# Optimization experiments

Hardware: AMD Instinct MI355X
Metric: run time of the kernel (lower is better)

## Reference

```python
import jax, jax.numpy as jnp
import numpy as np

DIM = 512
HEADS = 8
DIM_HEAD = 64
INNER = HEADS * DIM_HEAD  # 512
SCALE = DIM_HEAD ** -0.5
LN_EPS = 1e-5


def setup_inputs() -> dict:
    key = jax.random.key(0)
    k1, k2, k3, k4 = jax.random.split(key, 4)
    b, p, n = 4, 64, 256
    x = jax.random.normal(k1, (b, p, n, DIM), dtype=jnp.float32)
    ln_g = jnp.ones((DIM,), jnp.float32)
    ln_b = jnp.zeros((DIM,), jnp.float32)
    # stored as [in, out] for x @ W
    w_qkv = jax.random.normal(k2, (DIM, 3 * INNER), jnp.float32) * (DIM ** -0.5)
    w_out = jax.random.normal(k3, (INNER, DIM), jnp.float32) * (INNER ** -0.5)
    b_out = jnp.zeros((DIM,), jnp.float32)
    return {"x": x, "ln_g": ln_g, "ln_b": ln_b, "w_qkv": w_qkv,
            "w_out": w_out, "b_out": b_out}


def reference(x, ln_g, ln_b, w_qkv, w_out, b_out):
    b, p, n, _ = x.shape
    # LayerNorm over last dim
    mu = jnp.mean(x, axis=-1, keepdims=True)
    var = jnp.mean(jnp.square(x - mu), axis=-1, keepdims=True)
    xn = (x - mu) * jax.lax.rsqrt(var + LN_EPS) * ln_g + ln_b
    # QKV projection (no bias)
    qkv = xn @ w_qkv                                   # [b,p,n,3*INNER]
    q, k, v = jnp.split(qkv, 3, axis=-1)
    def to_heads(t):
        return t.reshape(b, p, n, HEADS, DIM_HEAD).transpose(0, 1, 3, 2, 4)
    q, k, v = to_heads(q), to_heads(k), to_heads(v)    # [b,p,h,n,d]
    dots = jnp.einsum('bphnd,bphmd->bphnm', q, k) * SCALE
    attn = jax.nn.softmax(dots, axis=-1)
    out = jnp.einsum('bphnm,bphmd->bphnd', attn, v)    # [b,p,h,n,d]
    out = out.transpose(0, 1, 3, 2, 4).reshape(b, p, n, INNER)
    return out @ w_out + b_out
```

## Files before the change

kernel.cpp:

```cpp
#include <hip/hip_runtime.h>
#include <stdint.h>

#define DIMD 512
#define HEADS 8
#define DHEAD 64
#define NSEQ 256
#define NGRP 256
#define NROWS (NGRP * NSEQ)
#define TRIPLE 1536
#define ATT_SCALE 0.125f

typedef float f32x4 __attribute__((ext_vector_type(4)));
typedef _Float16 half8 __attribute__((ext_vector_type(8)));
typedef _Float16 half4 __attribute__((ext_vector_type(4)));

#define GLD16(gp, lp) __builtin_amdgcn_global_load_lds( \
    (const __attribute__((address_space(1))) void*)(gp), \
    (__attribute__((address_space(3))) void*)(lp), 16, 0, 0)

__global__ __launch_bounds__(256) void k_wconv(const float* __restrict__ wq,
                                               const float* __restrict__ wo,
                                               _Float16* __restrict__ wtq,
                                               _Float16* __restrict__ wto) {
  int id = blockIdx.x * 256 + threadIdx.x;
  if (id < DIMD * TRIPLE) {
    int k = id / TRIPLE, n = id % TRIPLE;
    wtq[n * DIMD + k] = (_Float16)wq[id];
  } else {
    int j = id - DIMD * TRIPLE;
    int k = j / DIMD, n = j % DIMD;
    wto[n * DIMD + k] = (_Float16)wo[j];
  }
}

__global__ __launch_bounds__(256) void k_ln(const float* __restrict__ x,
                                            const float* __restrict__ g,
                                            const float* __restrict__ b,
                                            _Float16* __restrict__ xn) {
  int row = blockIdx.x * 4 + (threadIdx.x >> 6);
  int lane = threadIdx.x & 63;
  const float* xr = x + (size_t)row * DIMD + lane * 8;
  float v[8];
  *(f32x4*)(v)     = *(const f32x4*)(xr);
  *(f32x4*)(v + 4) = *(const f32x4*)(xr + 4);
  float s = 0.f, ss = 0.f;
#pragma unroll
  for (int j = 0; j < 8; ++j) { s += v[j]; ss += v[j] * v[j]; }
#pragma unroll
  for (int m = 1; m < 64; m <<= 1) { s += __shfl_xor(s, m); ss += __shfl_xor(ss, m); }
  float mean = s * (1.f / DIMD);
  float var  = ss * (1.f / DIMD) - mean * mean;
  float rstd = rsqrtf(var + 1e-5f);
  const float* gp = g + lane * 8;
  const float* bp = b + lane * 8;
  half8 o;
#pragma unroll
  for (int j = 0; j < 8; ++j) o[j] = (_Float16)((v[j] - mean) * rstd * gp[j] + bp[j]);
  *(half8*)(xn + (size_t)row * DIMD + lane * 8) = o;
}

template <int N, int LDA, bool WITH_BIAS>
__global__ __launch_bounds__(256, 2) void k_gemm(const _Float16* __restrict__ A,
                                                 const _Float16* __restrict__ BT,
                                                 _Float16* __restrict__ Ch,
                                                 float* __restrict__ Cf,
                                                 const float* __restrict__ bias) {
  constexpr int NT = N / 128;
  int mt = blockIdx.x / NT, nt = blockIdx.x % NT;
  int m0 = mt * 128, n0 = nt * 128;
  int tid = threadIdx.x, lane = tid & 63, w = tid >> 6;
  int wr = w >> 1, wc = w & 1;
  int l15 = lane & 15, lg = lane >> 4;
  __shared__ _Float16 Asm[128 * 64];
  __shared__ _Float16 Bsm[128 * 64];
  f32x4 acc[4][4] = {};
  const int rA = lane >> 3;
  const int cA = (lane & 7) * 8;

  for (int ks = 0; ks < 8; ++ks) {
    int k0 = ks * 64;
#pragma unroll
    for (int i = 0; i < 4; ++i) {
      int r0 = w * 32 + i * 8;
      GLD16(A  + (size_t)(m0 + r0 + rA) * LDA + k0 + cA, &Asm[r0 * 64]);
      GLD16(BT + (size_t)(n0 + r0 + rA) * 512 + k0 + cA, &Bsm[r0 * 64]);
    }
    __syncthreads();
#pragma unroll
    for (int kk = 0; kk < 2; ++kk) {
      int co = kk * 32 + lg * 8;
      half8 a[4], b[4];
#pragma unroll
      for (int m = 0; m < 4; ++m) a[m] = *(const half8*)&Asm[(wr * 64 + m * 16 + l15) * 64 + co];
#pragma unroll
      for (int n = 0; n < 4; ++n) b[n] = *(const half8*)&Bsm[(wc * 64 + n * 16 + l15) * 64 + co];
#pragma unroll
      for (int m = 0; m < 4; ++m)
#pragma unroll
        for (int n = 0; n < 4; ++n)
          acc[m][n] = __builtin_amdgcn_mfma_f32_16x16x32_f16(a[m], b[n], acc[m][n], 0, 0, 0);
    }
    __syncthreads();
  }

  int rowb = m0 + wr * 64 + lg * 4;
  int colb = n0 + wc * 64 + l15;
  float bb[4];
  if constexpr (WITH_BIAS) {
#pragma unroll
    for (int n = 0; n < 4; ++n) bb[n] = bias[colb + n * 16];
  }
#pragma unroll
  for (int m = 0; m < 4; ++m)
#pragma unroll
    for (int n = 0; n < 4; ++n)
#pragma unroll
      for (int r = 0; r < 4; ++r) {
        size_t idx = (size_t)(rowb + m * 16 + r) * N + colb + n * 16;
        if constexpr (WITH_BIAS)
          Cf[idx] = acc[m][n][r] + bb[n];
        else
          Ch[idx] = (_Float16)acc[m][n][r];
      }
}

__global__ __launch_bounds__(256, 2) void k_attn(_Float16* __restrict__ qkv) {
  int g = blockIdx.x >> 3, h = blockIdx.x & 7;
  int tid = threadIdx.x, lane = tid & 63, w = tid >> 6;
  int l15 = lane & 15, lg = lane >> 4;
  __shared__ _Float16 Kt[64 * 72];
  __shared__ _Float16 Vt[64 * 72];
  __shared__ _Float16 Pl[4][64 * 72];
  const size_t base = (size_t)g * NSEQ * TRIPLE;

  half8 qf[4][2];
#pragma unroll
  for (int nq = 0; nq < 4; ++nq)
#pragma unroll
    for (int kd = 0; kd < 2; ++kd)
      qf[nq][kd] = *(const half8*)&qkv[base + (size_t)(w * 64 + nq * 16 + l15) * TRIPLE
                                       + h * 64 + kd * 32 + lg * 8];

  f32x4 oacc[4][4] = {};
  float mrun[4], lrun[4];
#pragma unroll
  for (int nq = 0; nq < 4; ++nq) { mrun[nq] = -3.0e38f; lrun[nq] = 0.f; }

  for (int kt = 0; kt < 4; ++kt) {
    __syncthreads();
#pragma unroll
    for (int i = 0; i < 2; ++i) {
      int idx = tid + i * 256;
      int key = idx >> 3, dh0 = (idx & 7) * 8;
      half8 kv = *(const half8*)&qkv[base + (size_t)(kt * 64 + key) * TRIPLE + 512 + h * 64 + dh0];
      *(half8*)&Kt[key * 72 + dh0] = kv;
      half8 vv = *(const half8*)&qkv[base + (size_t)(kt * 64 + key) * TRIPLE + 1024 + h * 64 + dh0];
#pragma unroll
      for (int j = 0; j < 8; ++j) Vt[(dh0 + j) * 72 + key] = vv[j];
    }
    __syncthreads();

    f32x4 st[4][4] = {};
#pragma unroll
    for (int kd = 0; kd < 2; ++kd) {
      int co = kd * 32 + lg * 8;
      half8 kf[4];
#pragma unroll
      for (int mk = 0; mk < 4; ++mk) kf[mk] = *(const half8*)&Kt[(mk * 16 + l15) * 72 + co];
#pragma unroll
      for (int mk = 0; mk < 4; ++mk)
#pragma unroll
        for (int nq = 0; nq < 4; ++nq)
          st[mk][nq] = __builtin_amdgcn_mfma_f32_16x16x32_f16(kf[mk], qf[nq][kd], st[mk][nq], 0, 0, 0);
    }

    float alpha[4];
#pragma unroll
    for (int nq = 0; nq < 4; ++nq) {
      float pm = -3.0e38f;
#pragma unroll
      for (int mk = 0; mk < 4; ++mk)
#pragma unroll
        for (int r = 0; r < 4; ++r) {
          st[mk][nq][r] *= ATT_SCALE;
          pm = fmaxf(pm, st[mk][nq][r]);
        }
      pm = fmaxf(pm, __shfl_xor(pm, 16));
      pm = fmaxf(pm, __shfl_xor(pm, 32));
      float mn = fmaxf(mrun[nq], pm);
      alpha[nq] = __expf(mrun[nq] - mn);
      mrun[nq] = mn;
      float ps = 0.f;
#pragma unroll
      for (int mk = 0; mk < 4; ++mk) {
        half4 p4;
#pragma unroll
        for (int r = 0; r < 4; ++r) {
          float e = __expf(st[mk][nq][r] - mn);
          ps += e;
          p4[r] = (_Float16)e;
        }
        *(half4*)&Pl[w][(nq * 16 + l15) * 72 + mk * 16 + lg * 4] = p4;
      }
      ps += __shfl_xor(ps, 16);
      ps += __shfl_xor(ps, 32);
      lrun[nq] = lrun[nq] * alpha[nq] + ps;
    }

#pragma unroll
    for (int mp = 0; mp < 4; ++mp)
#pragma unroll
      for (int r = 0; r < 4; ++r) {
        float av = __shfl(alpha[mp], lg * 4 + r);
#pragma unroll
        for (int nd = 0; nd < 4; ++nd) oacc[mp][nd][r] *= av;
      }

    __syncthreads();

#pragma unroll
    for (int kp = 0; kp < 2; ++kp) {
      int co = kp * 32 + lg * 8;
      half8 pf[4], vf[4];
#pragma unroll
      for (int mp = 0; mp < 4; ++mp) pf[mp] = *(const half8*)&Pl[w][(mp * 16 + l15) * 72 + co];
#pragma unroll
      for (int nd = 0; nd < 4; ++nd) vf[nd] = *(const half8*)&Vt[(nd * 16 + l15) * 72 + co];
#pragma unroll
      for (int mp = 0; mp < 4; ++mp)
#pragma unroll
        for (int nd = 0; nd < 4; ++nd)
          oacc[mp][nd] = __builtin_amdgcn_mfma_f32_16x16x32_f16(pf[mp], vf[nd], oacc[mp][nd], 0, 0, 0);
    }
  }

#pragma unroll
  for (int mp = 0; mp < 4; ++mp)
#pragma unroll
    for (int r = 0; r < 4; ++r) {
      float li = 1.f / __shfl(lrun[mp], lg * 4 + r);
      int q = w * 64 + mp * 16 + lg * 4 + r;
#pragma unroll
      for (int nd = 0; nd < 4; ++nd)
        qkv[base + (size_t)q * TRIPLE + h * 64 + nd * 16 + l15] =
            (_Float16)(oacc[mp][nd][r] * li);
    }
}

extern "C" void kernel_launch(void* const* d_in, const int* in_sizes, int n_in,
                              void* d_out, int out_size, void* d_ws, size_t ws_size,
                              hipStream_t stream) {
  const float* x     = (const float*)d_in[0];
  const float* ln_g  = (const float*)d_in[1];
  const float* ln_b  = (const float*)d_in[2];
  const float* w_qkv = (const float*)d_in[3];
  const float* w_out = (const float*)d_in[4];
  const float* b_out = (const float*)d_in[5];

  char* ws = (char*)d_ws;
  _Float16* qkv = (_Float16*)ws;
  _Float16* wtq = (_Float16*)(ws + 201326592ull);
  _Float16* wto = (_Float16*)(ws + 201326592ull + 1572864ull);
  _Float16* xn  = (_Float16*)d_out;
  float* out    = (float*)d_out;

  k_wconv<<<4096, 256, 0, stream>>>(w_qkv, w_out, wtq, wto);
  k_ln<<<16384, 256, 0, stream>>>(x, ln_g, ln_b, xn);
  k_gemm<TRIPLE, DIMD, false><<<6144, 256, 0, stream>>>(xn, wtq, qkv, nullptr, nullptr);
  k_attn<<<2048, 256, 0, stream>>>(qkv);
  k_gemm<DIMD, TRIPLE, true><<<2048, 256, 0, stream>>>(qkv, wto, nullptr, out, b_out);
}
```

Measured before the change: 332.1 us.

## Add 256x256 eight-wave pipelined GEMM for QKV projection with XCD-aware block swizzle

Replaces the QKV projection GEMM with a new kernel that uses 256x256 tiles, 512 threads, double-buffered LDS filled by direct global-to-LDS loads in half-tile chunks, XOR-swizzled LDS layout, and interleaved MFMA quadrants with setprio. Block indices are remapped so consecutive tiles land on the same XCD for L2 reuse, and the same remap is applied to the output projection GEMM. The aim is higher arithmetic intensity and overlap of loads with MFMA work. In exchange it uses 128KB of LDS and more registers per block, and the output stores remain scalar half writes.

Measured after the change: 306.7 us. 7.6% less time.

```diff
diff --git a/kernel.cpp b/kernel.cpp
--- a/kernel.cpp
+++ b/kernel.cpp
@@ -6,7 +6,6 @@
 #define DHEAD 64
 #define NSEQ 256
 #define NGRP 256
-#define NROWS (NGRP * NSEQ)
 #define TRIPLE 1536
 #define ATT_SCALE 0.125f
 
@@ -17,6 +16,8 @@
 #define GLD16(gp, lp) __builtin_amdgcn_global_load_lds( \
     (const __attribute__((address_space(1))) void*)(gp), \
     (__attribute__((address_space(3))) void*)(lp), 16, 0, 0)
+#define BAR() __builtin_amdgcn_s_barrier()
+#define VMW(n) asm volatile("s_waitcnt vmcnt(" #n ")" ::: "memory")
 
 __global__ __launch_bounds__(256) void k_wconv(const float* __restrict__ wq,
                                                const float* __restrict__ wo,
@@ -59,6 +60,122 @@
   *(half8*)(xn + (size_t)row * DIMD + lane * 8) = o;
 }
 
+template <int N, int LDA>
+__global__ __launch_bounds__(512, 2) void k_gemm8(const _Float16* __restrict__ A,
+                                                  const _Float16* __restrict__ BT,
+                                                  _Float16* __restrict__ C) {
+  constexpr int NT = N / 256;
+  constexpr int NWG = 256 * NT;
+  constexpr int CPX = NWG / 8;
+  int b = blockIdx.x;
+  int logical = (b & 7) * CPX + (b >> 3);
+  int mt = logical / NT, nt = logical % NT;
+  int m0 = mt * 256, n0 = nt * 256;
+
+  int tid = threadIdx.x, lane = tid & 63, w = tid >> 6;
+  int wrow = w >> 2, wcol = w & 3;
+  int l15 = lane & 15, lg = lane >> 4;
+  const int sr = lane >> 3;
+  const int ss = lane & 7;
+
+  __shared__ _Float16 S[65536];
+
+  f32x4 acc[8][4] = {};
+  half8 af[4][2], bf0[2][2], bf1[2][2];
+
+  auto stageA = [&](int d, int kt, int hf) {
+#pragma unroll
+    for (int cc = 0; cc < 2; ++cc) {
+      int rbase = cc * 128 + hf * 64 + w * 8;
+      const _Float16* g = A + (size_t)(m0 + rbase + sr) * LDA + kt * 64 + (ss ^ sr) * 8;
+      _Float16* l = &S[d * 32768 + rbase * 64];
+      GLD16(g, l);
+    }
+  };
+  auto stageB = [&](int d, int kt, int hf) {
+#pragma unroll
+    for (int cc = 0; cc < 2; ++cc) {
+      int i = cc * 64 + w * 8;
+      int rbase = (i >> 5) * 64 + hf * 32 + (i & 31);
+      const _Float16* g = BT + (size_t)(n0 + rbase + sr) * 512 + kt * 64 + (ss ^ sr) * 8;
+      _Float16* l = &S[d * 32768 + 16384 + rbase * 64];
+      GLD16(g, l);
+    }
+  };
+  auto loadA = [&](int c, int mh) {
+#pragma unroll
+    for (int mf = 0; mf < 4; ++mf) {
+      int row = wrow * 128 + mh * 64 + mf * 16 + l15;
+#pragma unroll
+      for (int kk = 0; kk < 2; ++kk) {
+        int byte = row * 128 + ((kk * 64 + lg * 16) ^ ((row & 7) << 4));
+        af[mf][kk] = *(const half8*)((const char*)&S[c * 32768] + byte);
+      }
+    }
+  };
+  auto loadB = [&](int c, int nh, half8 (&bf)[2][2]) {
+#pragma unroll
+    for (int nf = 0; nf < 2; ++nf) {
+      int row = wcol * 64 + nh * 32 + nf * 16 + l15;
+#pragma unroll
+      for (int kk = 0; kk < 2; ++kk) {
+        int byte = row * 128 + ((kk * 64 + lg * 16) ^ ((row & 7) << 4));
+        bf[nf][kk] = *(const half8*)((const char*)&S[c * 32768 + 16384] + byte);
+      }
+    }
+  };
+  auto quad = [&](int mh, int nh, half8 (&bf)[2][2]) {
+    __builtin_amdgcn_s_setprio(1);
+#pragma unroll
+    for (int mf = 0; mf < 4; ++mf)
+#pragma unroll
+      for (int nf = 0; nf < 2; ++nf)
+#pragma unroll
+        for (int kk = 0; kk < 2; ++kk)
+          acc[mh * 4 + mf][nh * 2 + nf] = __builtin_amdgcn_mfma_f32_16x16x32_f16(
+              af[mf][kk], bf[nf][kk], acc[mh * 4 + mf][nh * 2 + nf], 0, 0, 0);
+    __builtin_amdgcn_s_setprio(0);
+  };
+
+  stageA(0, 0, 0); stageB(0, 0, 0); stageB(0, 0, 1); stageA(0, 0, 1);
+  VMW(4); BAR();
+
+  for (int t = 0; t < 7; ++t) {
+    int c = t & 1, d = c ^ 1;
+    loadA(c, 0); loadB(c, 0, bf0);
+    stageA(d, t + 1, 0);
+    BAR(); quad(0, 0, bf0); VMW(4); BAR();
+    loadB(c, 1, bf1);
+    stageB(d, t + 1, 0);
+    BAR(); quad(0, 1, bf1); VMW(4); BAR();
+    loadA(c, 1);
+    stageB(d, t + 1, 1);
+    BAR(); quad(1, 0, bf0); BAR();
+    stageA(d, t + 1, 1);
+    BAR(); quad(1, 1, bf1); VMW(4); BAR();
+  }
+  {
+    loadA(1, 0); loadB(1, 0, bf0);
+    BAR(); quad(0, 0, bf0); VMW(2); BAR();
+    loadB(1, 1, bf1);
+    BAR(); quad(0, 1, bf1); VMW(0); BAR();
+    loadA(1, 1);
+    BAR(); quad(1, 0, bf0); BAR();
+    BAR(); quad(1, 1, bf1); BAR();
+  }
+
+#pragma unroll
+  for (int mq = 0; mq < 8; ++mq)
+#pragma unroll
+    for (int nq = 0; nq < 4; ++nq)
+#pragma unroll
+      for (int r = 0; r < 4; ++r) {
+        int row = m0 + wrow * 128 + (mq >> 2) * 64 + (mq & 3) * 16 + lg * 4 + r;
+        int col = n0 + wcol * 64 + (nq >> 1) * 32 + (nq & 1) * 16 + l15;
+        C[(size_t)row * N + col] = (_Float16)acc[mq][nq][r];
+      }
+}
+
 template <int N, int LDA, bool WITH_BIAS>
 __global__ __launch_bounds__(256, 2) void k_gemm(const _Float16* __restrict__ A,
                                                  const _Float16* __restrict__ BT,
@@ -66,7 +183,10 @@
                                                  float* __restrict__ Cf,
                                                  const float* __restrict__ bias) {
   constexpr int NT = N / 128;
-  int mt = blockIdx.x / NT, nt = blockIdx.x % NT;
+  constexpr int NWG = 512 * NT;
+  constexpr int CPX = NWG / 8;
+  int bsw = (blockIdx.x & 7) * CPX + (blockIdx.x >> 3);
+  int mt = bsw / NT, nt = bsw % NT;
   int m0 = mt * 128, n0 = nt * 128;
   int tid = threadIdx.x, lane = tid & 63, w = tid >> 6;
   int wr = w >> 1, wc = w & 1;
@@ -266,7 +386,7 @@
 
   k_wconv<<<4096, 256, 0, stream>>>(w_qkv, w_out, wtq, wto);
   k_ln<<<16384, 256, 0, stream>>>(x, ln_g, ln_b, xn);
-  k_gemm<TRIPLE, DIMD, false><<<6144, 256, 0, stream>>>(xn, wtq, qkv, nullptr, nullptr);
+  k_gemm8<TRIPLE, DIMD><<<1536, 512, 0, stream>>>(xn, wtq, qkv);
   k_attn<<<2048, 256, 0, stream>>>(qkv);
   k_gemm<DIMD, TRIPLE, true><<<2048, 256, 0, stream>>>(qkv, wto, nullptr, out, b_out);
 }
```
